# Kernel optimization log

Measured on AMD Instinct MI355X. Metric: run time of the kernel, lower is better.

The kernel has to match this reference:

```python
import jax, jax.numpy as jnp
import numpy as np

N = 100000
E = 1600000
IN_DIM, HID, H_IN, OUT_DIM, H_OUT = 128, 32, 2, 1, 1
NEG_SLOPE = 0.2


def gat_conv(x, W, a_src, a_dst, b, src, dst, concat):
    """PyG-style GATConv. x:[N,F_in], W:[F_in,H*C], a_*:[H,C], b:[H*C] or [C]."""
    H, C = a_src.shape
    h = (x @ W).reshape(N, H, C)
    asrc = jnp.einsum('nhc,hc->nh', h, a_src)   # [N,H]
    adst = jnp.einsum('nhc,hc->nh', h, a_dst)   # [N,H]
    e = jax.nn.leaky_relu(asrc[src] + adst[dst], NEG_SLOPE)  # [E',H]
    # segment softmax over incoming edges of each destination node
    m = jax.ops.segment_max(e, dst, num_segments=N)
    p = jnp.exp(e - m[dst])
    s = jax.ops.segment_sum(p, dst, num_segments=N)
    alpha = p / s[dst]                           # [E',H]
    out = jax.ops.segment_sum(alpha[:, :, None] * h[src], dst, num_segments=N)  # [N,H,C]
    out = out.reshape(N, H * C) if concat else out.mean(axis=1)
    return out + b


def setup_inputs() -> dict:
    key = jax.random.key(0)
    ks = jax.random.split(key, 16)
    def glorot(k, shape):
        fan = sum(shape[-2:]) if len(shape) > 1 else shape[-1]
        return jax.random.normal(k, shape, jnp.float32) * (2.0 / fan) ** 0.5
    node_attrs = jax.random.normal(ks[0], (N, IN_DIM), jnp.float32)
    edge_index = jax.random.randint(ks[1], (2, E), 0, N, jnp.int64 if jax.config.jax_enable_x64 else jnp.int32)
    params = {
        'W_in':  glorot(ks[2], (IN_DIM, H_IN * HID)),
        'a_src_in': glorot(ks[3], (H_IN, HID)),
        'a_dst_in': glorot(ks[4], (H_IN, HID)),
        'b_in':  jnp.zeros((H_IN * HID,), jnp.float32),
        'W_mid': glorot(ks[5], (H_IN * HID, H_IN * HID)),
        'a_src_mid': glorot(ks[6], (H_IN, HID)),
        'a_dst_mid': glorot(ks[7], (H_IN, HID)),
        'b_mid': jnp.zeros((H_IN * HID,), jnp.float32),
        'W_out': glorot(ks[8], (H_IN * HID, H_OUT * OUT_DIM)),
        'a_src_out': glorot(ks[9], (H_OUT, OUT_DIM)),
        'a_dst_out': glorot(ks[10], (H_OUT, OUT_DIM)),
        'b_out': jnp.zeros((OUT_DIM,), jnp.float32),
    }
    return {'node_attrs': node_attrs, 'edge_index': edge_index, **params}


def reference(node_attrs, edge_index,
              W_in, a_src_in, a_dst_in, b_in,
              W_mid, a_src_mid, a_dst_mid, b_mid,
              W_out, a_src_out, a_dst_out, b_out):
    # add self loops (PyG GATConv default add_self_loops=True)
    loops = jnp.arange(N, dtype=edge_index.dtype)
    src = jnp.concatenate([edge_index[0], loops])
    dst = jnp.concatenate([edge_index[1], loops])

    x = gat_conv(node_attrs, W_in, a_src_in, a_dst_in, b_in, src, dst, True)
    initial_x = x
    x = jax.nn.elu(x)
    for _ in range(6):  # conv_mid reused 6 times with SHARED weights, as in source
        x = gat_conv(x, W_mid, a_src_mid, a_dst_mid, b_mid, src, dst, True) + initial_x
        x = jax.nn.elu(x)
    x = gat_conv(x, W_out, a_src_out, a_dst_out, b_out, src, dst, False)
    return jax.nn.sigmoid(x)
```

## Files before the change

kernel.cpp:

```cpp
#include <hip/hip_runtime.h>
#include <hip/hip_fp16.h>
#include <cmath>

#define NN 100000
#define EE 1600000
#define TOTE (EE + NN)
#define SHIFT 10
#define NBUK 98
#define CAPB 18432
#define SLACK 5632
#define SPAN (TOTE + NBUK * SLACK)
#define PCAP2 40


typedef _Float16 half8_t __attribute__((ext_vector_type(8)));
typedef _Float16 half4_t __attribute__((ext_vector_type(4)));
typedef float float4_t __attribute__((ext_vector_type(4)));

__device__ __forceinline__ float lrelu(float v) { return v > 0.f ? v : 0.2f * v; }

__global__ __launch_bounds__(256) void binA(const int* __restrict__ src, const int* __restrict__ dst,
                                            int* __restrict__ gcur, int* __restrict__ region) {
    __shared__ int cnt[NBUK], gbase[NBUK], pos[NBUK];
    int t = threadIdx.x;
    if (t < NBUK) cnt[t] = 0;
    __syncthreads();
    const int CH = (TOTE + gridDim.x - 1) / gridDim.x;
    int lo = blockIdx.x * CH;
    int hi = lo + CH; if (hi > TOTE) hi = TOTE;
    for (int e = lo + t; e < hi; e += 256) {
        int d = (e < EE) ? dst[e] : (e - EE);
        atomicAdd(&cnt[d >> SHIFT], 1);
    }
    __syncthreads();
    if (t < NBUK) {
        gbase[t] = atomicAdd(&gcur[t], cnt[t]);
        pos[t] = 0;
    }
    __syncthreads();
    for (int e = lo + t; e < hi; e += 256) {
        int s, d;
        if (e < EE) { s = src[e]; d = dst[e]; }
        else        { s = e - EE; d = s; }
        int b = d >> SHIFT;
        int k = atomicAdd(&pos[b], 1);
        region[(size_t)b * CAPB + gbase[b] + k] = (s << SHIFT) | (d & 1023);
    }
}

__global__ __launch_bounds__(1024) void binB(const int* __restrict__ region, const int* __restrict__ gcur,
                                             int2* __restrict__ rng, int* __restrict__ esrc) {
    __shared__ int ncur[1024];
    __shared__ int wsum[16];
    __shared__ int sg[NBUK];
    __shared__ int sBase;
    int b = blockIdx.x, t = threadIdx.x;
    int n0 = b << SHIFT;
    if (t < NBUK) sg[t] = gcur[t];
    ncur[t] = 0;
    __syncthreads();
    if (t == 0) {
        int run = 0;
        for (int bb = 0; bb < b; ++bb) run += sg[bb] + SLACK;
        sBase = run;
    }
    int cntE = gcur[b];
    const int* reg = region + (size_t)b * CAPB;
    __syncthreads();
    for (int i = t; i < cntE; i += 1024)
        atomicAdd(&ncur[reg[i] & 1023], 1);
    int base = sBase;
    __syncthreads();
    int v = ncur[t];
    int vp = (v + 7) & ~7;
    __syncthreads();
    int incl = vp;
    for (int off = 1; off < 64; off <<= 1) {
        int u = __shfl_up(incl, off);
        if ((t & 63) >= off) incl += u;
    }
    if ((t & 63) == 63) wsum[t >> 6] = incl;
    __syncthreads();
    if (t < 16) {
        int w = wsum[t];
        int winc = w;
        for (int off = 1; off < 16; off <<= 1) {
            int u = __shfl_up(winc, off);
            if (t >= off) winc += u;
        }
        wsum[t] = winc - w;
    }
    __syncthreads();
    int excl = incl - vp + wsum[t >> 6];
    int start = base + excl;
    int n = n0 + t;
    if (n < NN) rng[n] = make_int2(start, v);
    ncur[t] = start;
    __syncthreads();
    for (int i = t; i < cntE; i += 1024) {
        int p = reg[i];
        int local = p & 1023;
        int k = atomicAdd(&ncur[local], 1);
        esrc[k] = p >> SHIFT;
    }
    __syncthreads();
    if (n < NN) {
        for (int k = start + v; k < start + vp; ++k) esrc[k] = 0;
    }
}

__global__ __launch_bounds__(256) void degHist(const int2* __restrict__ rng, int* __restrict__ hist) {
    __shared__ int cnt[64];
    int t = threadIdx.x;
    if (t < 64) cnt[t] = 0;
    __syncthreads();
    int n = blockIdx.x * 256 + t;
    if (n < NN) {
        int d = rng[n].y; if (d > 63) d = 63;
        atomicAdd(&cnt[d], 1);
    }
    __syncthreads();
    if (t < 64 && cnt[t]) atomicAdd(&hist[t], cnt[t]);
}

__global__ void degScan(const int* __restrict__ hist, int* __restrict__ off) {
    int t = threadIdx.x;
    int v = hist[t];
    int incl = v;
    for (int o = 1; o < 64; o <<= 1) {
        int u = __shfl_up(incl, o);
        if (t >= o) incl += u;
    }
    off[t] = incl - v;
}

__global__ __launch_bounds__(256) void degSort(const int2* __restrict__ rng, int* __restrict__ off,
                                               int* __restrict__ perm) {
    __shared__ int cnt[64], base[64], pos[64];
    int t = threadIdx.x;
    if (t < 64) cnt[t] = 0;
    __syncthreads();
    int n = blockIdx.x * 256 + t;
    int d = 63;
    if (n < NN) {
        d = rng[n].y; if (d > 63) d = 63;
        atomicAdd(&cnt[d], 1);
    }
    __syncthreads();
    if (t < 64) { base[t] = atomicAdd(&off[t], cnt[t]); pos[t] = 0; }
    __syncthreads();
    if (n < NN) {
        int k = atomicAdd(&pos[d], 1);
        perm[base[d] + k] = n;
    }
}

__global__ void prepW(const float* __restrict__ Wg, _Float16* __restrict__ Wp) {
    int t = threadIdx.x;
    for (int i = t; i < 64 * 72; i += 256) {
        int row = i / 72, col = i - row * 72;
        _Float16 v = (_Float16)0.f;
        if (col < 64) {
            int k = (col & 3) * 16 + (col >> 2);
            v = (_Float16)Wg[k * 64 + row];
        }
        Wp[i] = v;
    }
}

template <int K, bool F32IN>
__global__ __launch_bounds__(256) void gemm_attn(const void* __restrict__ Xv, const float* __restrict__ W,
                                                 const float* __restrict__ a_src, const float* __restrict__ a_dst,
                                                 _Float16* __restrict__ H, float* __restrict__ asrc,
                                                 float* __restrict__ adst) {
    __shared__ _Float16 wt[64][K + 8];
    int t = threadIdx.x;
    for (int it = 0; it < K / 16; ++it) {
        int idx4 = it * 256 + t;
        int k = idx4 >> 4;
        int n4 = (idx4 * 4) & 63;
        int ks = F32IN ? k : ((k & 15) * 4 + (k >> 4));
        float4 v = *(const float4*)(W + (size_t)idx4 * 4);
        wt[n4 + 0][ks] = (_Float16)v.x;
        wt[n4 + 1][ks] = (_Float16)v.y;
        wt[n4 + 2][ks] = (_Float16)v.z;
        wt[n4 + 3][ks] = (_Float16)v.w;
    }
    __syncthreads();

    int row0 = blockIdx.x * 64;
    int wr = (t >> 6) * 16;
    int lane = t & 63;
    int m = lane & 15;
    int q = lane >> 4;

    int rowA = row0 + wr + m;
    if (rowA >= NN) rowA = NN - 1;

    float4_t acc[4] = { {0,0,0,0}, {0,0,0,0}, {0,0,0,0}, {0,0,0,0} };
#pragma unroll
    for (int kc = 0; kc < K / 32; ++kc) {
        half8_t av;
        if (F32IN) {
            const float* xrow = (const float*)Xv + (size_t)rowA * K + q * 8;
            float4 u0 = *(const float4*)(xrow + kc * 32);
            float4 u1 = *(const float4*)(xrow + kc * 32 + 4);
            av[0] = (_Float16)u0.x; av[1] = (_Float16)u0.y;
            av[2] = (_Float16)u0.z; av[3] = (_Float16)u0.w;
            av[4] = (_Float16)u1.x; av[5] = (_Float16)u1.y;
            av[6] = (_Float16)u1.z; av[7] = (_Float16)u1.w;
        } else {
            const _Float16* xrow = (const _Float16*)Xv + (size_t)rowA * K + q * 8;
            av = *(const half8_t*)(xrow + kc * 32);
        }
#pragma unroll
        for (int c = 0; c < 4; ++c) {
            half8_t bv = *(const half8_t*)&wt[c * 16 + m][kc * 32 + q * 8];
            acc[c] = __builtin_amdgcn_mfma_f32_16x16x32_f16(av, bv, acc[c], 0, 0, 0);
        }
    }

#pragma unroll
    for (int r = 0; r < 4; ++r) {
        int row = row0 + wr + q * 4 + r;
        if (row < NN) {
            half4_t hv = { (_Float16)acc[0][r], (_Float16)acc[1][r],
                           (_Float16)acc[2][r], (_Float16)acc[3][r] };
            *(half4_t*)(H + (size_t)row * 64 + m * 4) = hv;
        }
    }

    float as0 = a_src[m], as1 = a_src[16 + m], as2 = a_src[32 + m], as3 = a_src[48 + m];
    float ad0 = a_dst[m], ad1 = a_dst[16 + m], ad2 = a_dst[32 + m], ad3 = a_dst[48 + m];
#pragma unroll
    for (int r = 0; r < 4; ++r) {
        float s0 = acc[0][r] * as0 + acc[1][r] * as1;
        float s1 = acc[2][r] * as2 + acc[3][r] * as3;
        float d0 = acc[0][r] * ad0 + acc[1][r] * ad1;
        float d1 = acc[2][r] * ad2 + acc[3][r] * ad3;
#pragma unroll
        for (int mk = 1; mk < 16; mk <<= 1) {
            s0 += __shfl_xor(s0, mk);
            s1 += __shfl_xor(s1, mk);
            d0 += __shfl_xor(d0, mk);
            d1 += __shfl_xor(d1, mk);
        }
        int row = row0 + wr + q * 4 + r;
        if (m == 0 && row < NN) {
            asrc[2 * row + 0] = s0;
            asrc[2 * row + 1] = s1;
            adst[2 * row + 0] = d0;
            adst[2 * row + 1] = d1;
        }
    }
}

struct Acc8 { float a[8]; float l0, l1; };

__device__ __forceinline__ void acc4(Acc8& A, float4 p0, float4 p1, float4 p2, float4 p3,
                                     half8_t h0, half8_t h1, half8_t h2, half8_t h3) {
    A.l0 += p0.x + p1.x + p2.x + p3.x;
    A.l1 += p0.y + p1.y + p2.y + p3.y;
#pragma unroll
    for (int q = 0; q < 8; ++q) {
        float w0 = (q & 2) ? p0.y : p0.x;
        float w1 = (q & 2) ? p1.y : p1.x;
        float w2 = (q & 2) ? p2.y : p2.x;
        float w3 = (q & 2) ? p3.y : p3.x;
        A.a[q] += w0 * (float)h0[q] + w1 * (float)h1[q]
                + w2 * (float)h2[q] + w3 * (float)h3[q];
    }
}

template <int MODE>
__global__ __launch_bounds__(256, 6) void edge_agg(const int* __restrict__ perm, const int2* __restrict__ rng,
                                                const int* __restrict__ esrc, const _Float16* __restrict__ h,
                                                const float* __restrict__ asrc, const float* __restrict__ adst,
                                                const float* __restrict__ bias, _Float16* __restrict__ ixbuf,
                                                const _Float16* __restrict__ Wp, const float* __restrict__ asg,
                                                const float* __restrict__ adg, _Float16* __restrict__ hN,
                                                float* __restrict__ asrcN, float* __restrict__ adstN,
                                                const float* __restrict__ Wo, const float* __restrict__ a_s,
                                                const float* __restrict__ a_d, float2* __restrict__ ho2,
                                                float* __restrict__ adst_o) {
    __shared__ float4 pLDS[4][8][PCAP2 + 1];
    int bid = gridDim.x - 1 - blockIdx.x;
    int tid = threadIdx.x;
    int wq = tid >> 6;
    int lane = tid & 63;
    int g = lane >> 3;
    int c8 = lane & 7;

    int n = perm[(bid * 4 + wq) * 8 + g];
    int2 r = rng[n];
    int start = r.x, deg = r.y;
    int vp = (deg + 3) & ~3;
    if (vp > PCAP2) vp = PCAP2;
    float2 ad = *(const float2*)(adst + 2 * (size_t)n);

    for (int j = c8; j < vp; j += 8) {
        float p0 = 0.f, p1 = 0.f;
        int s = 0;
        if (j < deg) {
            s = esrc[start + j];
            float2 as = *(const float2*)(asrc + 2 * (size_t)s);
            p0 = __expf(fminf(lrelu(as.x + ad.x), 60.f));
            p1 = __expf(fminf(lrelu(as.y + ad.y), 60.f));
        }
        pLDS[wq][g][j] = make_float4(p0, p1, __int_as_float(s), 0.f);
    }

    float bi[8];
#pragma unroll
    for (int q = 0; q < 8; ++q) bi[q] = bias[(q & 3) * 16 + 2 * c8 + (q >> 2)];
    half8_t iv = {};
    if constexpr (MODE != 0) iv = *(const half8_t*)(ixbuf + (size_t)n * 64 + 8 * c8);
    float wo[8];
    float as0o = 0.f, ad0o = 0.f;
    if constexpr (MODE == 2) {
#pragma unroll
        for (int q = 0; q < 8; ++q) wo[q] = Wo[(q & 3) * 16 + 2 * c8 + (q >> 2)];
        as0o = a_s[0]; ad0o = a_d[0];
    }

    const float4* pb = &pLDS[wq][g][0];
    const _Float16* hb = h + 8 * c8;
    Acc8 A = {};
    float4 pc0 = pb[0], pc1 = pb[1], pc2 = pb[2], pc3 = pb[3];
    half8_t hc0 = *(const half8_t*)(hb + ((size_t)__float_as_int(pc0.z) << 6));
    half8_t hc1 = *(const half8_t*)(hb + ((size_t)__float_as_int(pc1.z) << 6));
    half8_t hc2 = *(const half8_t*)(hb + ((size_t)__float_as_int(pc2.z) << 6));
    half8_t hc3 = *(const half8_t*)(hb + ((size_t)__float_as_int(pc3.z) << 6));
    for (int j = 4; j < vp; j += 4) {
        float4 pn0 = pb[j], pn1 = pb[j + 1], pn2 = pb[j + 2], pn3 = pb[j + 3];
        acc4(A, pc0, pc1, pc2, pc3, hc0, hc1, hc2, hc3);
        half8_t hn0 = *(const half8_t*)(hb + ((size_t)__float_as_int(pn0.z) << 6));
        half8_t hn1 = *(const half8_t*)(hb + ((size_t)__float_as_int(pn1.z) << 6));
        half8_t hn2 = *(const half8_t*)(hb + ((size_t)__float_as_int(pn2.z) << 6));
        half8_t hn3 = *(const half8_t*)(hb + ((size_t)__float_as_int(pn3.z) << 6));
        pc0 = pn0; pc1 = pn1; pc2 = pn2; pc3 = pn3;
        hc0 = hn0; hc1 = hn1; hc2 = hn2; hc3 = hn3;
    }
    acc4(A, pc0, pc1, pc2, pc3, hc0, hc1, hc2, hc3);

    float inv0 = 1.f / A.l0, inv1 = 1.f / A.l1;
    float t[8];
#pragma unroll
    for (int q = 0; q < 8; ++q) t[q] = A.a[q] * ((q & 2) ? inv1 : inv0) + bi[q];
    if constexpr (MODE == 0) {
        half8_t o;
#pragma unroll
        for (int q = 0; q < 8; ++q) o[q] = (_Float16)t[q];
        *(half8_t*)(ixbuf + (size_t)n * 64 + 8 * c8) = o;
    } else {
#pragma unroll
        for (int q = 0; q < 8; ++q) t[q] += (float)iv[q];
    }
#pragma unroll
    for (int q = 0; q < 8; ++q) t[q] = t[q] > 0.f ? t[q] : __expf(t[q]) - 1.f;

    if constexpr (MODE != 2) {
        _Float16* xs = (_Float16*)&pLDS[wq][0][0];
        half8_t xv;
#pragma unroll
        for (int q = 0; q < 8; ++q) xv[q] = (_Float16)t[q];
        *(half8_t*)(xs + g * 72 + 8 * c8) = xv;
        int m = lane & 15, qq = lane >> 4;
        half8_t bf0[4], bf1[4];
#pragma unroll
        for (int c = 0; c < 4; ++c) {
            const _Float16* wrow = Wp + (c * 16 + m) * 72 + qq * 8;
            bf0[c] = *(const half8_t*)(wrow);
            bf1[c] = *(const half8_t*)(wrow + 32);
        }
        const _Float16* xrow = xs + (m & 7) * 72 + qq * 8;
        half8_t a0 = *(const half8_t*)(xrow);
        half8_t a1 = *(const half8_t*)(xrow + 32);
        float4_t ag[4] = { {0,0,0,0}, {0,0,0,0}, {0,0,0,0}, {0,0,0,0} };
#pragma unroll
        for (int c = 0; c < 4; ++c) {
            ag[c] = __builtin_amdgcn_mfma_f32_16x16x32_f16(a0, bf0[c], ag[c], 0, 0, 0);
            ag[c] = __builtin_amdgcn_mfma_f32_16x16x32_f16(a1, bf1[c], ag[c], 0, 0, 0);
        }
        int base = (bid * 4 + wq) * 8;
#pragma unroll
        for (int rr = 0; rr < 4; ++rr) {
            if (qq < 2) {
                int nr = perm[base + qq * 4 + rr];
                half4_t hv = { (_Float16)ag[0][rr], (_Float16)ag[1][rr],
                               (_Float16)ag[2][rr], (_Float16)ag[3][rr] };
                *(half4_t*)(hN + (size_t)nr * 64 + m * 4) = hv;
            }
        }
        float gs0 = asg[m], gs1 = asg[16 + m], gs2 = asg[32 + m], gs3 = asg[48 + m];
        float gd0 = adg[m], gd1 = adg[16 + m], gd2 = adg[32 + m], gd3 = adg[48 + m];
#pragma unroll
        for (int rr = 0; rr < 4; ++rr) {
            float s0 = ag[0][rr] * gs0 + ag[1][rr] * gs1;
            float s1 = ag[2][rr] * gs2 + ag[3][rr] * gs3;
            float d0 = ag[0][rr] * gd0 + ag[1][rr] * gd1;
            float d1 = ag[2][rr] * gd2 + ag[3][rr] * gd3;
#pragma unroll
            for (int mk = 1; mk < 16; mk <<= 1) {
                s0 += __shfl_xor(s0, mk);
                s1 += __shfl_xor(s1, mk);
                d0 += __shfl_xor(d0, mk);
                d1 += __shfl_xor(d1, mk);
            }
            if (m == 0 && qq < 2) {
                int nr = perm[base + qq * 4 + rr];
                asrcN[2 * nr + 0] = s0;
                asrcN[2 * nr + 1] = s1;
                adstN[2 * nr + 0] = d0;
                adstN[2 * nr + 1] = d1;
            }
        }
    } else {
        float v = 0.f;
#pragma unroll
        for (int q = 0; q < 8; ++q) v += t[q] * wo[q];
        v += __shfl_xor(v, 1);
        v += __shfl_xor(v, 2);
        v += __shfl_xor(v, 4);
        if (c8 == 0) {
            ho2[n] = make_float2(v, v * as0o);
            adst_o[n] = v * ad0o;
        }
    }
}

__global__ __launch_bounds__(256) void edge_agg_out(const int* __restrict__ perm, const int2* __restrict__ rng,
                                                    const int* __restrict__ esrc, const float2* __restrict__ ho2,
                                                    const float* __restrict__ adst_o, const float* __restrict__ b_out,
                                                    float* __restrict__ out) {
    int bid = gridDim.x - 1 - blockIdx.x;
    int wq = threadIdx.x >> 6;
    int lane = threadIdx.x & 63;
    int g = lane >> 3;
    int c8 = lane & 7;
    int n = perm[(bid * 4 + wq) * 8 + g];
    int2 r = rng[n];
    float adv = adst_o[n];
    float l = 0.f, acc = 0.f;
    for (int j = c8; j < r.y; j += 8) {
        int s = esrc[r.x + j];
        float2 v = ho2[s];
        float p = __expf(fminf(lrelu(v.y + adv), 60.f));
        l += p;
        acc = fmaf(p, v.x, acc);
    }
    l += __shfl_xor(l, 1); acc += __shfl_xor(acc, 1);
    l += __shfl_xor(l, 2); acc += __shfl_xor(acc, 2);
    l += __shfl_xor(l, 4); acc += __shfl_xor(acc, 4);
    if (c8 == 0) out[n] = 1.f / (1.f + __expf(-(acc / l + b_out[0])));
}

extern "C" void kernel_launch(void* const* d_in, const int* in_sizes, int n_in,
                              void* d_out, int out_size, void* d_ws, size_t ws_size,
                              hipStream_t stream) {
    const float* node_attrs = (const float*)d_in[0];
    const int*   edge_index = (const int*)d_in[1];
    const float* W_in      = (const float*)d_in[2];
    const float* a_src_in  = (const float*)d_in[3];
    const float* a_dst_in  = (const float*)d_in[4];
    const float* b_in      = (const float*)d_in[5];
    const float* W_mid     = (const float*)d_in[6];
    const float* a_src_mid = (const float*)d_in[7];
    const float* a_dst_mid = (const float*)d_in[8];
    const float* b_mid     = (const float*)d_in[9];
    const float* W_out     = (const float*)d_in[10];
    const float* a_src_out = (const float*)d_in[11];
    const float* a_dst_out = (const float*)d_in[12];
    const float* b_out     = (const float*)d_in[13];
    float* out = (float*)d_out;

    const int* srcArr = edge_index;
    const int* dstArr = edge_index + EE;

    char* w = (char*)d_ws;
    auto alloc = [&](size_t bytes) { void* p = (void*)w; w += (bytes + 255) & ~(size_t)255; return p; };
    int2*  rng        = (int2*)alloc((size_t)NN * 8);
    int*   gcur       = (int*)alloc((size_t)NBUK * 4);
    int*   region     = (int*)alloc((size_t)NBUK * CAPB * 4);
    int*   esrc       = (int*)alloc((size_t)SPAN * 4);
    _Float16* hA      = (_Float16*)alloc((size_t)NN * 64 * 2);
    _Float16* hB      = (_Float16*)alloc((size_t)NN * 64 * 2);
    _Float16* ixbuf   = (_Float16*)alloc((size_t)NN * 64 * 2);
    float* asA        = (float*)alloc((size_t)NN * 2 * 4);
    float* adA        = (float*)alloc((size_t)NN * 2 * 4);
    float* asB        = (float*)alloc((size_t)NN * 2 * 4);
    float* adB        = (float*)alloc((size_t)NN * 2 * 4);
    float2* ho2       = (float2*)alloc((size_t)NN * 8);
    float* adst_o     = (float*)alloc((size_t)NN * 4);
    int*   perm       = (int*)alloc((size_t)NN * 4);
    int*   hist      = (int*)alloc(64 * 4);
    int*   off        = (int*)alloc(64 * 4);
    _Float16* wperm   = (_Float16*)alloc((size_t)64 * 72 * 2);

    hipMemsetAsync(gcur, 0, NBUK * 4, stream);
    hipMemsetAsync(hist, 0, 64 * 4, stream);
    binA<<<256, 256, 0, stream>>>(srcArr, dstArr, gcur, region);
    binB<<<NBUK, 1024, 0, stream>>>(region, gcur, rng, esrc);

    int nBlk = (NN + 255) / 256;
    degHist<<<nBlk, 256, 0, stream>>>(rng, hist);
    degScan<<<1, 64, 0, stream>>>(hist, off);
    degSort<<<nBlk, 256, 0, stream>>>(rng, off, perm);

    prepW<<<1, 256, 0, stream>>>(W_mid, wperm);

    int gemmBlocks = (NN + 63) / 64;
    int aggBlocks = NN / 32;

    gemm_attn<128, true><<<gemmBlocks, 256, 0, stream>>>(node_attrs, W_in, a_src_in, a_dst_in, hA, asA, adA);

    edge_agg<0><<<aggBlocks, 256, 0, stream>>>(perm, rng, esrc, hA, asA, adA, b_in, ixbuf,
                                               wperm, a_src_mid, a_dst_mid, hB, asB, adB,
                                               nullptr, nullptr, nullptr, nullptr, nullptr);

    for (int l = 0; l < 5; ++l) {
        _Float16* hs = (l & 1) ? hA : hB;  float* ass = (l & 1) ? asA : asB;  float* ads = (l & 1) ? adA : adB;
        _Float16* hd = (l & 1) ? hB : hA;  float* asd = (l & 1) ? asB : asA;  float* add = (l & 1) ? adB : adA;
        edge_agg<1><<<aggBlocks, 256, 0, stream>>>(perm, rng, esrc, hs, ass, ads, b_mid, ixbuf,
                                                   wperm, a_src_mid, a_dst_mid, hd, asd, add,
                                                   nullptr, nullptr, nullptr, nullptr, nullptr);
    }
    edge_agg<2><<<aggBlocks, 256, 0, stream>>>(perm, rng, esrc, hA, asA, adA, b_mid, ixbuf,
                                               nullptr, nullptr, nullptr, nullptr, nullptr, nullptr,
                                               W_out, a_src_out, a_dst_out, ho2, adst_o);

    edge_agg_out<<<aggBlocks, 256, 0, stream>>>(perm, rng, esrc, ho2, adst_o, b_out, out);
}
```

Baseline: 522.0 us.

## Renumber nodes into degree-sorted slot order for mid and output layers

Builds an inverse permutation and rewrites edge source indices and per-node ranges into degree-sorted slot space. Layer outputs (h, attention scalars, residual buffer) are then stored and read by slot rather than by original node id, so the mid and output aggregation kernels skip the perm indirection. Contiguous slot storage should make per-node writes and reads coalesced. The cost is two extra setup kernels, a second copy of the edge array, and extra workspace.

```diff
diff --git a/kernel.cpp b/kernel.cpp
--- a/kernel.cpp
+++ b/kernel.cpp
@@ -11,7 +11,6 @@
 #define SLACK 5632
 #define SPAN (TOTE + NBUK * SLACK)
 #define PCAP2 40
-
 
 typedef _Float16 half8_t __attribute__((ext_vector_type(8)));
 typedef _Float16 half4_t __attribute__((ext_vector_type(4)));
@@ -152,6 +151,26 @@
     if (n < NN) {
         int k = atomicAdd(&pos[d], 1);
         perm[base[d] + k] = n;
+    }
+}
+
+__global__ __launch_bounds__(256) void mkInvRng(const int* __restrict__ perm, const int2* __restrict__ rng,
+                                                int* __restrict__ inv, int2* __restrict__ rng2) {
+    int i = blockIdx.x * 256 + threadIdx.x;
+    if (i < NN) {
+        int p = perm[i];
+        inv[p] = i;
+        rng2[i] = rng[p];
+    }
+}
+
+__global__ __launch_bounds__(256) void xlat(const int* __restrict__ esrc, const int* __restrict__ inv,
+                                            int* __restrict__ esrc2) {
+    int k = blockIdx.x * 256 + threadIdx.x;
+    if (k < SPAN) {
+        unsigned v = (unsigned)esrc[k];
+        if (v >= NN) v = 0;
+        esrc2[k] = inv[v];
     }
 }
 
@@ -272,9 +291,9 @@
     }
 }
 
-template <int MODE>
-__global__ __launch_bounds__(256, 6) void edge_agg(const int* __restrict__ perm, const int2* __restrict__ rng,
-                                                const int* __restrict__ esrc, const _Float16* __restrict__ h,
+template <int MODE, bool SLOT>
+__global__ __launch_bounds__(256, 6) void edge_agg(const int* __restrict__ perm, const int2* __restrict__ rngP,
+                                                const int* __restrict__ esrcP, const _Float16* __restrict__ h,
                                                 const float* __restrict__ asrc, const float* __restrict__ adst,
                                                 const float* __restrict__ bias, _Float16* __restrict__ ixbuf,
                                                 const _Float16* __restrict__ Wp, const float* __restrict__ asg,
@@ -291,18 +310,20 @@
     int g = lane >> 3;
     int c8 = lane & 7;
 
-    int n = perm[(bid * 4 + wq) * 8 + g];
-    int2 r = rng[n];
+    int slot = (bid * 4 + wq) * 8 + g;
+    int mn;
+    if constexpr (SLOT) mn = slot; else mn = perm[slot];
+    int2 r = rngP[mn];
     int start = r.x, deg = r.y;
     int vp = (deg + 3) & ~3;
     if (vp > PCAP2) vp = PCAP2;
-    float2 ad = *(const float2*)(adst + 2 * (size_t)n);
+    float2 ad = *(const float2*)(adst + 2 * (size_t)mn);
 
     for (int j = c8; j < vp; j += 8) {
         float p0 = 0.f, p1 = 0.f;
         int s = 0;
         if (j < deg) {
-            s = esrc[start + j];
+            s = esrcP[start + j];
             float2 as = *(const float2*)(asrc + 2 * (size_t)s);
             p0 = __expf(fminf(lrelu(as.x + ad.x), 60.f));
             p1 = __expf(fminf(lrelu(as.y + ad.y), 60.f));
@@ -314,7 +335,7 @@
 #pragma unroll
     for (int q = 0; q < 8; ++q) bi[q] = bias[(q & 3) * 16 + 2 * c8 + (q >> 2)];
     half8_t iv = {};
-    if constexpr (MODE != 0) iv = *(const half8_t*)(ixbuf + (size_t)n * 64 + 8 * c8);
+    if constexpr (MODE != 0) iv = *(const half8_t*)(ixbuf + (size_t)slot * 64 + 8 * c8);
     float wo[8];
     float as0o = 0.f, ad0o = 0.f;
     if constexpr (MODE == 2) {
@@ -351,7 +372,7 @@
         half8_t o;
 #pragma unroll
         for (int q = 0; q < 8; ++q) o[q] = (_Float16)t[q];
-        *(half8_t*)(ixbuf + (size_t)n * 64 + 8 * c8) = o;
+        *(half8_t*)(ixbuf + (size_t)slot * 64 + 8 * c8) = o;
     } else {
 #pragma unroll
         for (int q = 0; q < 8; ++q) t[q] += (float)iv[q];
@@ -386,7 +407,7 @@
 #pragma unroll
         for (int rr = 0; rr < 4; ++rr) {
             if (qq < 2) {
-                int nr = perm[base + qq * 4 + rr];
+                int nr = base + qq * 4 + rr;
                 half4_t hv = { (_Float16)ag[0][rr], (_Float16)ag[1][rr],
                                (_Float16)ag[2][rr], (_Float16)ag[3][rr] };
                 *(half4_t*)(hN + (size_t)nr * 64 + m * 4) = hv;
@@ -408,7 +429,7 @@
                 d1 += __shfl_xor(d1, mk);
             }
             if (m == 0 && qq < 2) {
-                int nr = perm[base + qq * 4 + rr];
+                int nr = base + qq * 4 + rr;
                 asrcN[2 * nr + 0] = s0;
                 asrcN[2 * nr + 1] = s1;
                 adstN[2 * nr + 0] = d0;
@@ -423,14 +444,14 @@
         v += __shfl_xor(v, 2);
         v += __shfl_xor(v, 4);
         if (c8 == 0) {
-            ho2[n] = make_float2(v, v * as0o);
-            adst_o[n] = v * ad0o;
-        }
-    }
-}
-
-__global__ __launch_bounds__(256) void edge_agg_out(const int* __restrict__ perm, const int2* __restrict__ rng,
-                                                    const int* __restrict__ esrc, const float2* __restrict__ ho2,
+            ho2[slot] = make_float2(v, v * as0o);
+            adst_o[slot] = v * ad0o;
+        }
+    }
+}
+
+__global__ __launch_bounds__(256) void edge_agg_out(const int* __restrict__ perm, const int2* __restrict__ rng2,
+                                                    const int* __restrict__ esrc2, const float2* __restrict__ ho2,
                                                     const float* __restrict__ adst_o, const float* __restrict__ b_out,
                                                     float* __restrict__ out) {
     int bid = gridDim.x - 1 - blockIdx.x;
@@ -438,12 +459,12 @@
     int lane = threadIdx.x & 63;
     int g = lane >> 3;
     int c8 = lane & 7;
-    int n = perm[(bid * 4 + wq) * 8 + g];
-    int2 r = rng[n];
-    float adv = adst_o[n];
+    int slot = (bid * 4 + wq) * 8 + g;
+    int2 r = rng2[slot];
+    float adv = adst_o[slot];
     float l = 0.f, acc = 0.f;
     for (int j = c8; j < r.y; j += 8) {
-        int s = esrc[r.x + j];
+        int s = esrc2[r.x + j];
         float2 v = ho2[s];
         float p = __expf(fminf(lrelu(v.y + adv), 60.f));
         l += p;
@@ -452,7 +473,7 @@
     l += __shfl_xor(l, 1); acc += __shfl_xor(acc, 1);
     l += __shfl_xor(l, 2); acc += __shfl_xor(acc, 2);
     l += __shfl_xor(l, 4); acc += __shfl_xor(acc, 4);
-    if (c8 == 0) out[n] = 1.f / (1.f + __expf(-(acc / l + b_out[0])));
+    if (c8 == 0) out[perm[slot]] = 1.f / (1.f + __expf(-(acc / l + b_out[0])));
 }
 
 extern "C" void kernel_launch(void* const* d_in, const int* in_sizes, int n_in,
@@ -480,9 +501,11 @@
     char* w = (char*)d_ws;
     auto alloc = [&](size_t bytes) { void* p = (void*)w; w += (bytes + 255) & ~(size_t)255; return p; };
     int2*  rng        = (int2*)alloc((size_t)NN * 8);
+    int2*  rng2       = (int2*)alloc((size_t)NN * 8);
     int*   gcur       = (int*)alloc((size_t)NBUK * 4);
     int*   region     = (int*)alloc((size_t)NBUK * CAPB * 4);
     int*   esrc       = (int*)alloc((size_t)SPAN * 4);
+    int*   esrc2      = (int*)alloc((size_t)SPAN * 4);
     _Float16* hA      = (_Float16*)alloc((size_t)NN * 64 * 2);
     _Float16* hB      = (_Float16*)alloc((size_t)NN * 64 * 2);
     _Float16* ixbuf   = (_Float16*)alloc((size_t)NN * 64 * 2);
@@ -493,7 +516,8 @@
     float2* ho2       = (float2*)alloc((size_t)NN * 8);
     float* adst_o     = (float*)alloc((size_t)NN * 4);
     int*   perm       = (int*)alloc((size_t)NN * 4);
-    int*   hist      = (int*)alloc(64 * 4);
+    int*   invp       = (int*)alloc((size_t)NN * 4);
+    int*   hist       = (int*)alloc(64 * 4);
     int*   off        = (int*)alloc(64 * 4);
     _Float16* wperm   = (_Float16*)alloc((size_t)64 * 72 * 2);
 
@@ -506,6 +530,8 @@
     degHist<<<nBlk, 256, 0, stream>>>(rng, hist);
     degScan<<<1, 64, 0, stream>>>(hist, off);
     degSort<<<nBlk, 256, 0, stream>>>(rng, off, perm);
+    mkInvRng<<<nBlk, 256, 0, stream>>>(perm, rng, invp, rng2);
+    xlat<<<(SPAN + 255) / 256, 256, 0, stream>>>(esrc, invp, esrc2);
 
     prepW<<<1, 256, 0, stream>>>(W_mid, wperm);
 
@@ -514,20 +540,20 @@
 
     gemm_attn<128, true><<<gemmBlocks, 256, 0, stream>>>(node_attrs, W_in, a_src_in, a_dst_in, hA, asA, adA);
 
-    edge_agg<0><<<aggBlocks, 256, 0, stream>>>(perm, rng, esrc, hA, asA, adA, b_in, ixbuf,
-                                               wperm, a_src_mid, a_dst_mid, hB, asB, adB,
-                                               nullptr, nullptr, nullptr, nullptr, nullptr);
+    edge_agg<0, false><<<aggBlocks, 256, 0, stream>>>(perm, rng, esrc, hA, asA, adA, b_in, ixbuf,
+                                                      wperm, a_src_mid, a_dst_mid, hB, asB, adB,
+                                                      nullptr, nullptr, nullptr, nullptr, nullptr);
 
     for (int l = 0; l < 5; ++l) {
         _Float16* hs = (l & 1) ? hA : hB;  float* ass = (l & 1) ? asA : asB;  float* ads = (l & 1) ? adA : adB;
         _Float16* hd = (l & 1) ? hB : hA;  float* asd = (l & 1) ? asB : asA;  float* add = (l & 1) ? adB : adA;
-        edge_agg<1><<<aggBlocks, 256, 0, stream>>>(perm, rng, esrc, hs, ass, ads, b_mid, ixbuf,
-                                                   wperm, a_src_mid, a_dst_mid, hd, asd, add,
-                                                   nullptr, nullptr, nullptr, nullptr, nullptr);
-    }
-    edge_agg<2><<<aggBlocks, 256, 0, stream>>>(perm, rng, esrc, hA, asA, adA, b_mid, ixbuf,
-                                               nullptr, nullptr, nullptr, nullptr, nullptr, nullptr,
-                                               W_out, a_src_out, a_dst_out, ho2, adst_o);
-
-    edge_agg_out<<<aggBlocks, 256, 0, stream>>>(perm, rng, esrc, ho2, adst_o, b_out, out);
-}
+        edge_agg<1, true><<<aggBlocks, 256, 0, stream>>>(perm, rng2, esrc2, hs, ass, ads, b_mid, ixbuf,
+                                                         wperm, a_src_mid, a_dst_mid, hd, asd, add,
+                                                         nullptr, nullptr, nullptr, nullptr, nullptr);
+    }
+    edge_agg<2, true><<<aggBlocks, 256, 0, stream>>>(perm, rng2, esrc2, hA, asA, adA, b_mid, ixbuf,
+                                                     nullptr, nullptr, nullptr, nullptr, nullptr, nullptr,
+                                                     W_out, a_src_out, a_dst_out, ho2, adst_o);
+
+    edge_agg_out<<<aggBlocks, 256, 0, stream>>>(perm, rng2, esrc2, ho2, adst_o, b_out, out);
+}
```

Result: no change. 512.6 us (-1.8%).
